# Performance work log

Hardware: AMD Instinct MI355X
Metric: run time of the kernel (lower is better)

Reference implementation:

```python
import jax, jax.numpy as jnp
import numpy as np

N = 50000
E = 800000
EQ = 200000
IN_DIM = 256
H1 = 256
H2 = 128
EA = 16


def _lrelu(x):
    return jax.nn.leaky_relu(x, negative_slope=0.01)


def gcn_conv(h, edge_index, W, b, num_nodes):
    # PyG GCNConv: add self-loops, symmetric normalization, out = A_hat (h W) + b
    row, col = edge_index[0], edge_index[1]
    loop = jnp.arange(num_nodes, dtype=row.dtype)
    row = jnp.concatenate([row, loop])
    col = jnp.concatenate([col, loop])
    deg = jax.ops.segment_sum(jnp.ones(row.shape[0], dtype=h.dtype), col, num_segments=num_nodes)
    dinv = jnp.where(deg > 0, jax.lax.rsqrt(deg), 0.0)
    norm = dinv[row] * dinv[col]                      # [E+N]
    hw = h @ W                                        # [N, out]
    msg = hw[row] * norm[:, None]                     # gather + scale
    out = jax.ops.segment_sum(msg, col, num_segments=num_nodes)
    return out + b


def gru_cell(x, h, Wih, Whh, bih, bhh):
    # torch.nn.GRUCell, gate order (r, z, n); Wih/Whh stored as [in, 3H]
    gi = x @ Wih + bih
    gh = h @ Whh + bhh
    ir, iz, inn = jnp.split(gi, 3, axis=1)
    hr, hz, hn = jnp.split(gh, 3, axis=1)
    r = jax.nn.sigmoid(ir + hr)
    z = jax.nn.sigmoid(iz + hz)
    n = jnp.tanh(inn + r * hn)
    return (1.0 - z) * n + z * h


def setup_inputs() -> dict:
    key = jax.random.key(0)
    ks = jax.random.split(key, 24)

    def gn(k, shape, scale=0.05):
        return (jax.random.normal(k, shape, dtype=jnp.float32) * scale)

    inp = {
        "x": jax.random.normal(ks[0], (N, IN_DIM), dtype=jnp.float32),
        "edge_index": jax.random.randint(ks[1], (2, E), 0, N, dtype=jnp.int32).astype(jnp.int64),
        "edge_label_index": jax.random.randint(ks[2], (2, EQ), 0, N, dtype=jnp.int32).astype(jnp.int64),
        "edge_attr": jax.random.normal(ks[3], (EQ, EA), dtype=jnp.float32),
        "prev1": jax.random.normal(ks[4], (N, H1), dtype=jnp.float32) * 0.1,
        "prev2": jax.random.normal(ks[5], (N, H2), dtype=jnp.float32) * 0.1,
        "pre1_W": gn(ks[6], (IN_DIM, 256)), "pre1_b": jnp.zeros((256,), jnp.float32),
        "pre2_W": gn(ks[7], (256, 128)), "pre2_b": jnp.zeros((128,), jnp.float32),
        "conv1_W": gn(ks[8], (128, H1)), "conv1_b": jnp.zeros((H1,), jnp.float32),
        "conv2_W": gn(ks[9], (H1, H2)), "conv2_b": jnp.zeros((H2,), jnp.float32),
        "gru1_Wih": gn(ks[10], (H1, 3 * H1)), "gru1_Whh": gn(ks[11], (H1, 3 * H1)),
        "gru1_bih": jnp.zeros((3 * H1,), jnp.float32), "gru1_bhh": jnp.zeros((3 * H1,), jnp.float32),
        "gru2_Wih": gn(ks[12], (H2, 3 * H2)), "gru2_Whh": gn(ks[13], (H2, 3 * H2)),
        "gru2_bih": jnp.zeros((3 * H2,), jnp.float32), "gru2_bhh": jnp.zeros((3 * H2,), jnp.float32),
        "post_W": gn(ks[14], (2 * H2 + EA, 1)), "post_b": jnp.zeros((1,), jnp.float32),
    }
    return inp


def reference(x, edge_index, edge_label_index, edge_attr, prev1, prev2,
              pre1_W, pre1_b, pre2_W, pre2_b,
              conv1_W, conv1_b, conv2_W, conv2_b,
              gru1_Wih, gru1_Whh, gru1_bih, gru1_bhh,
              gru2_Wih, gru2_Whh, gru2_bih, gru2_bhh,
              post_W, post_b):
    num_nodes = x.shape[0]
    # dense preprocessing (dropout p=0.0 -> identity)
    h = _lrelu(x @ pre1_W + pre1_b)
    h = _lrelu(h @ pre2_W + pre2_b)          # [N,128]
    # GCN layer 1 + GRU update with previous embeddings
    h = _lrelu(gcn_conv(h, edge_index, conv1_W, conv1_b, num_nodes))
    h = gru_cell(h, prev1, gru1_Wih, gru1_Whh, gru1_bih, gru1_bhh)
    emb1 = h
    # GCN layer 2 + GRU update
    h = _lrelu(gcn_conv(h, edge_index, conv2_W, conv2_b, num_nodes))
    h = gru_cell(h, prev2, gru2_Wih, gru2_Whh, gru2_bih, gru2_bhh)
    emb2 = h
    # edge-level prediction: gather endpoints, concat with edge_attr, linear
    h_src = h[edge_label_index[0]]
    h_dst = h[edge_label_index[1]]
    combined = jnp.concatenate([h_src, h_dst, edge_attr], axis=1)  # [Eq, 2*H2+EA]
    scores = (combined @ post_W + post_b).reshape(-1)              # [Eq]
    return (scores, emb1, emb2)
```

## Files before the change

kernel.cpp:

```cpp
#include <hip/hip_runtime.h>
#include <hip/hip_bf16.h>

#define DEVFN __device__ __forceinline__

constexpr int NN = 50000;
constexpr int NE = 800000;
constexpr int NQ = 200000;
constexpr long MP = 50048;

typedef __attribute__((ext_vector_type(8))) short bf16x8;
typedef __attribute__((ext_vector_type(2))) short s16x2;
typedef __attribute__((ext_vector_type(2))) float f32x2;
typedef __attribute__((ext_vector_type(4))) float f32x4;
typedef __attribute__((address_space(1))) const void gv_t;
typedef __attribute__((address_space(3))) void lv_t;

DEVFN float lrelu(float x) { return x > 0.f ? x : 0.01f * x; }
DEVFN float sigmoidf(float x) { return 1.f / (1.f + __expf(-x)); }
DEVFN float tanh_fast(float x) {
    float xc = fminf(fmaxf(x, -15.f), 15.f);
    float t = __expf(2.f * xc);
    return (t - 1.f) / (t + 1.f);
}

DEVFN short f2b(float v) {
    __hip_bfloat16 h = __float2bfloat16(v);
    return *reinterpret_cast<short*>(&h);
}
DEVFN float b2f(short s) {
    union { unsigned u; float f; } z;
    z.u = ((unsigned)(unsigned short)s) << 16;
    return z.f;
}
DEVFN void gld16(const void* g, void* l) {
    __builtin_amdgcn_global_load_lds((gv_t*)g, (lv_t*)l, 16, 0, 0);
}

#define WAITV4 asm volatile("s_waitcnt vmcnt(4)" ::: "memory")
#define WAITV0 asm volatile("s_waitcnt vmcnt(0)" ::: "memory")
#define CFENCE asm volatile("" ::: "memory")

DEVFN void swz_rc(int d, int nwg, int NC, int& rw, int& cs) {
    int q0 = nwg >> 3, rr = nwg & 7;
    int xcd = d & 7, idx = d >> 3;
    int w = (xcd < rr ? xcd * (q0 + 1) : rr * (q0 + 1) + (xcd - rr) * q0) + idx;
    rw = w / NC;
    cs = w - rw * NC;
}

template <int H>
DEVFN float gruw_val(const float* Wih, const float* Whh, int i) {
    constexpr int K2 = 2 * H, W3 = 3 * H;
    int np = i / K2, k = i % K2;
    int g16 = np >> 6, chunk = (np >> 4) & 3, cl = np & 15;
    int c = g16 * 16 + cl;
    if (chunk == 0) return (k < H) ? Wih[(long)k * W3 + c] : Whh[(long)(k - H) * W3 + c];
    if (chunk == 1) return (k < H) ? Wih[(long)k * W3 + H + c] : Whh[(long)(k - H) * W3 + H + c];
    if (chunk == 2) return (k < H) ? Wih[(long)k * W3 + 2 * H + c] : 0.f;
    return (k < H) ? 0.f : Whh[(long)(k - H) * W3 + 2 * H + c];
}

__global__ void prep_all(const float* __restrict__ x, const float* __restrict__ prev1,
                         const float* __restrict__ pre1W, const float* __restrict__ pre2W,
                         const float* __restrict__ conv1W, const float* __restrict__ conv2W,
                         const float* __restrict__ g1ih, const float* __restrict__ g1hh,
                         const float* __restrict__ g2ih, const float* __restrict__ g2hh,
                         short* __restrict__ xb, short* __restrict__ AP1,
                         short* __restrict__ pre1T, short* __restrict__ pre2T,
                         short* __restrict__ conv1T, short* __restrict__ conv2T,
                         short* __restrict__ W1g1, short* __restrict__ W1g2) {
    long i = (long)blockIdx.x * 256 + threadIdx.x;
    if (i < MP * 256) {
        xb[i] = (i < (long)NN * 256) ? f2b(x[i]) : (short)0;
        return;
    }
    i -= MP * 256;
    if (i < (long)NN * 256) {
        long r = i >> 8; int c = (int)(i & 255);
        AP1[r * 512 + 256 + c] = f2b(prev1[i]);
        return;
    }
    i -= (long)NN * 256;
    if (i < 65536) { int ii = (int)i, n = ii >> 8, k = ii & 255; pre1T[ii] = f2b(pre1W[k * 256 + n]); return; }
    i -= 65536;
    if (i < 32768) { int ii = (int)i, n = ii >> 8, k = ii & 255; pre2T[ii] = f2b(pre2W[k * 128 + n]); return; }
    i -= 32768;
    if (i < 32768) { int ii = (int)i, n = ii >> 7, k = ii & 127; conv1T[ii] = f2b(conv1W[k * 256 + n]); return; }
    i -= 32768;
    if (i < 32768) { int ii = (int)i, n = ii >> 8, k = ii & 255; conv2T[ii] = f2b(conv2W[k * 128 + n]); return; }
    i -= 32768;
    if (i < 524288) { W1g1[i] = f2b(gruw_val<256>(g1ih, g1hh, (int)i)); return; }
    i -= 524288;
    if (i < 131072) W1g2[i] = f2b(gruw_val<128>(g2ih, g2hh, (int)i));
}

template <int EPI, int K>
__global__ __launch_bounds__(256)
void gemm_mfma(const short* __restrict__ A, const short* __restrict__ Bt,
               const float* __restrict__ bias,
               short* __restrict__ Cb, int obS, int NC, int nwg) {
    constexpr int NS = K / 32;
    __shared__ alignas(16) short As[3][4096];
    __shared__ alignas(16) short Bs[3][4096];
    const int tid = threadIdx.x;
    const int lane = tid & 63, w = tid >> 6;
    const int wr = w >> 1, wc = w & 1;
    int rw, cs;
    swz_rc(blockIdx.x, nwg, NC, rw, cs);
    const long row0 = (long)rw * 128;
    const long col0 = (long)cs * 128;

    f32x4 acc[4][4] = {};

    const int kcs = ((tid & 3) ^ ((tid >> 3) & 3)) * 8;
    const short* gA = A + (row0 + (tid >> 2)) * (long)K + kcs;
    const short* gB = Bt + (col0 + (tid >> 2)) * (long)K + kcs;
    const long half = 64 * (long)K;

    auto stage = [&](int b, int k0) {
        gld16(gA + k0, &As[b][tid * 8]);
        gld16(gA + half + k0, &As[b][2048 + tid * 8]);
        gld16(gB + k0, &Bs[b][tid * 8]);
        gld16(gB + half + k0, &Bs[b][2048 + tid * 8]);
    };

    stage(0, 0);
    stage(1, 32);
    const int l15 = lane & 15;
    const int kq = ((lane >> 4) ^ ((l15 >> 1) & 3)) * 8;
#pragma unroll
    for (int t = 0; t < NS; ++t) {
        if (t + 1 < NS) { WAITV4; } else { WAITV0; }
        __builtin_amdgcn_s_barrier();
        CFENCE;
        if (t + 2 < NS) stage((t + 2) % 3, (t + 2) * 32);
        const int cur = t % 3;
        bf16x8 af[4], bfr[4];
#pragma unroll
        for (int i = 0; i < 4; ++i)
            af[i] = *(const bf16x8*)&As[cur][(wr * 64 + i * 16 + l15) * 32 + kq];
#pragma unroll
        for (int j = 0; j < 4; ++j)
            bfr[j] = *(const bf16x8*)&Bs[cur][(wc * 64 + j * 16 + l15) * 32 + kq];
#pragma unroll
        for (int i = 0; i < 4; ++i)
#pragma unroll
            for (int j = 0; j < 4; ++j)
                acc[i][j] = __builtin_amdgcn_mfma_f32_16x16x32_bf16(af[i], bfr[j], acc[i][j], 0, 0, 0);
    }

    const int cr = (lane >> 4) * 4, cc = lane & 15;
#pragma unroll
    for (int i = 0; i < 4; ++i) {
#pragma unroll
        for (int j = 0; j < 4; ++j) {
            const long col = col0 + wc * 64 + j * 16 + cc;
            float bv = (EPI == 1) ? bias[col] : 0.f;
#pragma unroll
            for (int r = 0; r < 4; ++r) {
                const long row = row0 + wr * 64 + i * 16 + cr + r;
                float v = acc[i][j][r];
                if (EPI == 1) v = lrelu(v + bv);
                Cb[row * obS + col] = f2b(v);
            }
        }
    }
}

template <int H, bool WRITEB>
__global__ __launch_bounds__(256)
void gru_wide(const short* __restrict__ AP, const short* __restrict__ W1,
              const float* __restrict__ prevf,
              const float* __restrict__ bih, const float* __restrict__ bhh,
              float* __restrict__ outF, short* __restrict__ outB, int M,
              int NC, int nwg) {
    constexpr int K2 = 2 * H;
    constexpr int NS = K2 / 32;
    __shared__ alignas(16) short As[3][4096];
    __shared__ alignas(16) short Bs[3][4096];
    const int tid = threadIdx.x;
    const int lane = tid & 63, w = tid >> 6;
    const int wr = w >> 1, wc = w & 1;
    int rw, cs;
    swz_rc(blockIdx.x, nwg, NC, rw, cs);
    const long row0 = (long)rw * 128;

    f32x4 acc[4][4] = {};

    const int kcs = ((tid & 3) ^ ((tid >> 3) & 3)) * 8;
    const short* gA = AP + (row0 + (tid >> 2)) * (long)K2 + kcs;
    const short* gB = W1 + ((long)cs * 128 + (tid >> 2)) * (long)K2 + kcs;
    const long half = 64 * (long)K2;

    auto stage = [&](int b, int k0) {
        gld16(gA + k0, &As[b][tid * 8]);
        gld16(gA + half + k0, &As[b][2048 + tid * 8]);
        gld16(gB + k0, &Bs[b][tid * 8]);
        gld16(gB + half + k0, &Bs[b][2048 + tid * 8]);
    };

    stage(0, 0);
    stage(1, 32);
    const int l15 = lane & 15;
    const int kq = ((lane >> 4) ^ ((l15 >> 1) & 3)) * 8;
#pragma unroll
    for (int t = 0; t < NS; ++t) {
        const bool lo = (t * 32 < H);
        if (t + 1 < NS) { WAITV4; } else { WAITV0; }
        __builtin_amdgcn_s_barrier();
        CFENCE;
        if (t + 2 < NS) stage((t + 2) % 3, (t + 2) * 32);
        const int cur = t % 3;
        bf16x8 af[4], bfr[4];
#pragma unroll
        for (int i = 0; i < 4; ++i)
            af[i] = *(const bf16x8*)&As[cur][(wr * 64 + i * 16 + l15) * 32 + kq];
#pragma unroll
        for (int j = 0; j < 4; ++j) {
            if ((j == 2 && !lo) || (j == 3 && lo)) continue;
            bfr[j] = *(const bf16x8*)&Bs[cur][(wc * 64 + j * 16 + l15) * 32 + kq];
        }
#pragma unroll
        for (int i = 0; i < 4; ++i)
#pragma unroll
            for (int j = 0; j < 4; ++j) {
                if ((j == 2 && !lo) || (j == 3 && lo)) continue;
                acc[i][j] = __builtin_amdgcn_mfma_f32_16x16x32_bf16(af[i], bfr[j], acc[i][j], 0, 0, 0);
            }
    }

    const int cr = (lane >> 4) * 4;
    const int c = cs * 32 + wc * 16 + (lane & 15);
    const float bsr = bih[c] + bhh[c];
    const float bsz = bih[H + c] + bhh[H + c];
    const float bin = bih[2 * H + c];
    const float bhn = bhh[2 * H + c];
#pragma unroll
    for (int i = 0; i < 4; ++i) {
#pragma unroll
        for (int r = 0; r < 4; ++r) {
            const long row = row0 + wr * 64 + i * 16 + cr + r;
            if (row >= M) continue;
            float rg = sigmoidf(acc[i][0][r] + bsr);
            float zg = sigmoidf(acc[i][1][r] + bsz);
            float ng = tanh_fast(acc[i][2][r] + bin + rg * (acc[i][3][r] + bhn));
            float o = (1.f - zg) * ng + zg * prevf[row * (long)H + c];
            outF[row * (long)H + c] = o;
            if (WRITEB) outB[row * (long)H + c] = f2b(o);
        }
    }
}

__global__ void cnt_kernel(const int* __restrict__ cols, int* __restrict__ cnt, int E) {
    int e = blockIdx.x * 256 + threadIdx.x;
    if (e < E) atomicAdd(&cnt[cols[e]], 1);
}

__global__ void scan1(const int* __restrict__ cnt, int* __restrict__ off,
                      int* __restrict__ bsum, float* __restrict__ dinv, int n) {
    __shared__ int sm[256];
    int i = blockIdx.x * 256 + threadIdx.x;
    int v = (i < n) ? cnt[i] : 0;
    if (i < n) dinv[i] = rsqrtf((float)v + 1.0f);
    sm[threadIdx.x] = v;
    __syncthreads();
    for (int s = 1; s < 256; s <<= 1) {
        int t = (threadIdx.x >= s) ? sm[threadIdx.x - s] : 0;
        __syncthreads();
        sm[threadIdx.x] += t;
        __syncthreads();
    }
    if (i < n) off[i + 1] = sm[threadIdx.x];
    if (threadIdx.x == 255) bsum[blockIdx.x] = sm[255];
}

__global__ void scan2(int* __restrict__ bsum, int nb) {
    __shared__ int sm[256];
    int v = (threadIdx.x < nb) ? bsum[threadIdx.x] : 0;
    sm[threadIdx.x] = v;
    __syncthreads();
    for (int s = 1; s < 256; s <<= 1) {
        int t = (threadIdx.x >= s) ? sm[threadIdx.x - s] : 0;
        __syncthreads();
        sm[threadIdx.x] += t;
        __syncthreads();
    }
    if (threadIdx.x < nb) bsum[threadIdx.x] = sm[threadIdx.x] - v;
}

__global__ void scan3(int* __restrict__ off, const int* __restrict__ bsum, int n) {
    int i = blockIdx.x * 256 + threadIdx.x;
    if (i < n) off[i + 1] += bsum[blockIdx.x];
    if (i == 0) off[0] = 0;
}

__global__ void fill_csr(const int* __restrict__ rows, const int* __restrict__ cols,
                         const float* __restrict__ dinv, const int* __restrict__ off,
                         int* __restrict__ cursor, int* __restrict__ srow,
                         float* __restrict__ snorm, int E) {
    int e = blockIdx.x * 256 + threadIdx.x;
    if (e >= E) return;
    int r = rows[e], c = cols[e];
    int p = off[c] + atomicAdd(&cursor[c], 1);
    srow[p] = r;
    snorm[p] = dinv[r] * dinv[c];
}

template <int OS, bool EPI, bool PREV>
__global__ __launch_bounds__(256)
void gather_agg(const short* __restrict__ hwb, const int* __restrict__ off,
                const int* __restrict__ srow, const float* __restrict__ snorm,
                const float* __restrict__ dinv, const float* __restrict__ bias,
                const float* __restrict__ prevf,
                short* __restrict__ aggb, int n) {
    constexpr int H = 128;
    int t = blockIdx.x * 256 + threadIdx.x;
    int c = t >> 6, l = t & 63;
    if (c >= n) return;
    const int fo = l * 2;
    float acc0, acc1;
    {
        float dd = dinv[c] * dinv[c];
        s16x2 v = *(const s16x2*)&hwb[(long)c * H + fo];
        acc0 = b2f(v[0]) * dd;
        acc1 = b2f(v[1]) * dd;
    }
    int e = off[c];
    const int e1 = off[c + 1];
    for (; e + 3 < e1; e += 4) {
        int r0 = srow[e], r1 = srow[e + 1], r2 = srow[e + 2], r3 = srow[e + 3];
        float n0 = snorm[e], n1 = snorm[e + 1], n2 = snorm[e + 2], n3 = snorm[e + 3];
        s16x2 v0 = *(const s16x2*)&hwb[(long)r0 * H + fo];
        s16x2 v1 = *(const s16x2*)&hwb[(long)r1 * H + fo];
        s16x2 v2 = *(const s16x2*)&hwb[(long)r2 * H + fo];
        s16x2 v3 = *(const s16x2*)&hwb[(long)r3 * H + fo];
        acc0 += b2f(v0[0]) * n0 + b2f(v1[0]) * n1 + b2f(v2[0]) * n2 + b2f(v3[0]) * n3;
        acc1 += b2f(v0[1]) * n0 + b2f(v1[1]) * n1 + b2f(v2[1]) * n2 + b2f(v3[1]) * n3;
    }
    for (; e < e1; ++e) {
        int r0 = srow[e];
        float n0 = snorm[e];
        s16x2 v0 = *(const s16x2*)&hwb[(long)r0 * H + fo];
        acc0 += b2f(v0[0]) * n0;
        acc1 += b2f(v0[1]) * n0;
    }
    s16x2 o;
    if (EPI) {
        o[0] = f2b(lrelu(acc0 + bias[fo]));
        o[1] = f2b(lrelu(acc1 + bias[fo + 1]));
    } else {
        o[0] = f2b(acc0);
        o[1] = f2b(acc1);
    }
    *(s16x2*)&aggb[(long)c * OS + fo] = o;
    if (PREV) {
        f32x2 p = *(const f32x2*)&prevf[(long)c * H + fo];
        s16x2 pb;
        pb[0] = f2b(p[0]);
        pb[1] = f2b(p[1]);
        *(s16x2*)&aggb[(long)c * OS + H + fo] = pb;
    }
}

__global__ void edge_score_b(const short* __restrict__ emb2b, const int* __restrict__ eli,
                             const float* __restrict__ ea, const float* __restrict__ pw,
                             const float* __restrict__ pb, float* __restrict__ scores, int Q) {
    int t = blockIdx.x * 256 + threadIdx.x;
    int e = t >> 6, l = t & 63;
    if (e >= Q) return;
    int s = eli[e], d = eli[Q + e];
    const int f = l * 2;
    s16x2 vs = *(const s16x2*)&emb2b[(long)s * 128 + f];
    s16x2 vd = *(const s16x2*)&emb2b[(long)d * 128 + f];
    float acc = b2f(vs[0]) * pw[f] + b2f(vs[1]) * pw[f + 1]
              + b2f(vd[0]) * pw[128 + f] + b2f(vd[1]) * pw[128 + f + 1];
    if (l < 16) acc += ea[(long)e * 16 + l] * pw[256 + l];
#pragma unroll
    for (int off = 32; off > 0; off >>= 1) acc += __shfl_down(acc, off);
    if (l == 0) scores[e] = acc + pb[0];
}


extern "C" void kernel_launch(void* const* d_in, const int* in_sizes, int n_in,
                              void* d_out, int out_size, void* d_ws, size_t ws_size,
                              hipStream_t stream) {
    const float* x       = (const float*)d_in[0];
    const int*   ei      = (const int*)d_in[1];
    const int*   eli     = (const int*)d_in[2];
    const float* eattr   = (const float*)d_in[3];
    const float* prev1   = (const float*)d_in[4];
    const float* prev2   = (const float*)d_in[5];
    const float* pre1_W  = (const float*)d_in[6];
    const float* pre1_b  = (const float*)d_in[7];
    const float* pre2_W  = (const float*)d_in[8];
    const float* pre2_b  = (const float*)d_in[9];
    const float* conv1_W = (const float*)d_in[10];
    const float* conv1_b = (const float*)d_in[11];
    const float* conv2_W = (const float*)d_in[12];
    const float* conv2_b = (const float*)d_in[13];
    const float* g1_Wih  = (const float*)d_in[14];
    const float* g1_Whh  = (const float*)d_in[15];
    const float* g1_bih  = (const float*)d_in[16];
    const float* g1_bhh  = (const float*)d_in[17];
    const float* g2_Wih  = (const float*)d_in[18];
    const float* g2_Whh  = (const float*)d_in[19];
    const float* g2_bih  = (const float*)d_in[20];
    const float* g2_bhh  = (const float*)d_in[21];
    const float* post_W  = (const float*)d_in[22];
    const float* post_b  = (const float*)d_in[23];

    float* out    = (float*)d_out;
    float* scores = out;
    float* emb1   = out + NQ;
    float* emb2   = emb1 + (long)NN * 256;

    char* ws = (char*)d_ws;
    const long S256 = MP * 256 * 2;
    const long S128 = MP * 128 * 2;
    short* R1  = (short*)ws;
    short* R2  = (short*)(ws + S256);
    short* R3  = (short*)(ws + 2 * S256);
    short* AP1 = (short*)(ws + 2 * S256 + S128);
    short* AP2 = R1;
    char*  wts = ws + 4 * S256 + S128;
    short* pre1T  = (short*)wts;
    short* pre2T  = pre1T + 256 * 256;
    short* conv1T = pre2T + 128 * 256;
    short* conv2T = conv1T + 256 * 128;
    short* W1g1   = conv2T + 128 * 256;
    short* W1g2   = W1g1 + 1024 * 512;
    float* dinv   = (float*)(W1g2 + 512 * 256);
    int*   cnt    = (int*)(dinv + NN);
    int*   cursor = cnt + NN;
    int*   off    = cursor + NN;
    int*   bsum   = off + NN + 1;
    int*   srow   = bsum + 256;
    float* snorm  = (float*)(srow + NE);

    const int* rows = ei;
    const int* cols = ei + NE;

    dim3 blk(256);
    const int NB = (NN + 255) / 256;

    const long PREP = MP * 256 + (long)NN * 256 + 65536 + 3 * 32768 + 524288 + 131072;
    prep_all<<<(int)((PREP + 255) / 256), blk, 0, stream>>>(
        x, prev1, pre1_W, pre2_W, conv1_W, conv2_W,
        g1_Wih, g1_Whh, g2_Wih, g2_Whh,
        R1, AP1, pre1T, pre2T, conv1T, conv2T, W1g1, W1g2);

    hipMemsetAsync(cnt, 0, 2 * NN * sizeof(int), stream);
    cnt_kernel<<<(NE + 255) / 256, blk, 0, stream>>>(cols, cnt, NE);
    scan1<<<NB, blk, 0, stream>>>(cnt, off, bsum, dinv, NN);
    scan2<<<1, blk, 0, stream>>>(bsum, NB);
    scan3<<<NB, blk, 0, stream>>>(off, bsum, NN);
    fill_csr<<<(NE + 255) / 256, blk, 0, stream>>>(rows, cols, dinv, off, cursor, srow, snorm, NE);

    gemm_mfma<1, 256><<<782, blk, 0, stream>>>(R1, pre1T, pre1_b, R2, 256, 2, 782);
    gemm_mfma<1, 256><<<391, blk, 0, stream>>>(R2, pre2T, pre2_b, R3, 128, 1, 391);

    gather_agg<128, false, false><<<(NN + 3) / 4, blk, 0, stream>>>(
        R3, off, srow, snorm, dinv, nullptr, nullptr, R1, NN);
    gemm_mfma<1, 128><<<782, blk, 0, stream>>>(R1, conv1T, conv1_b, AP1, 512, 2, 782);

    gru_wide<256, true><<<3128, blk, 0, stream>>>(AP1, W1g1, prev1, g1_bih, g1_bhh,
                                                  emb1, R2, NN, 8, 3128);

    gemm_mfma<0, 256><<<391, blk, 0, stream>>>(R2, conv2T, nullptr, R3, 128, 1, 391);

    gather_agg<256, true, true><<<(NN + 3) / 4, blk, 0, stream>>>(
        R3, off, srow, snorm, dinv, conv2_b, prev2, AP2, NN);

    gru_wide<128, true><<<1564, blk, 0, stream>>>(AP2, W1g2, prev2, g2_bih, g2_bhh,
                                                  emb2, R3, NN, 4, 1564);

    edge_score_b<<<NQ / 4, blk, 0, stream>>>(R3, eli, eattr, post_W, post_b, scores, NQ);
}
```

Baseline: 459.3 us.

## Precompute per-node post-linear dots and fold edge-degree counting into prep kernel

Edge scoring is split in two. A per-node pass computes the two dot products of emb2 with the src and dst halves of post_W, and a light per-edge kernel then adds the edge_attr dot and looks up two scalars instead of gathering two 128-wide rows per query edge. The degree-count atomics are also merged into the prep_all kernel, with the memset moved before it, which removes one launch. The cost is an extra pass over all nodes and two small workspace arrays. Since 200k query edges over 50k nodes means rows are re-gathered about eight times, the per-node dots should reduce gather traffic.

```diff
diff --git a/kernel.cpp b/kernel.cpp
--- a/kernel.cpp
+++ b/kernel.cpp
@@ -65,6 +65,7 @@
                          const float* __restrict__ conv1W, const float* __restrict__ conv2W,
                          const float* __restrict__ g1ih, const float* __restrict__ g1hh,
                          const float* __restrict__ g2ih, const float* __restrict__ g2hh,
+                         const int* __restrict__ cols, int* __restrict__ cnt,
                          short* __restrict__ xb, short* __restrict__ AP1,
                          short* __restrict__ pre1T, short* __restrict__ pre2T,
                          short* __restrict__ conv1T, short* __restrict__ conv2T,
@@ -81,6 +82,8 @@
         return;
     }
     i -= (long)NN * 256;
+    if (i < NE) { atomicAdd(&cnt[cols[i]], 1); return; }
+    i -= NE;
     if (i < 65536) { int ii = (int)i, n = ii >> 8, k = ii & 255; pre1T[ii] = f2b(pre1W[k * 256 + n]); return; }
     i -= 65536;
     if (i < 32768) { int ii = (int)i, n = ii >> 8, k = ii & 255; pre2T[ii] = f2b(pre2W[k * 128 + n]); return; }
@@ -249,11 +252,6 @@
             if (WRITEB) outB[row * (long)H + c] = f2b(o);
         }
     }
-}
-
-__global__ void cnt_kernel(const int* __restrict__ cols, int* __restrict__ cnt, int E) {
-    int e = blockIdx.x * 256 + threadIdx.x;
-    if (e < E) atomicAdd(&cnt[cols[e]], 1);
 }
 
 __global__ void scan1(const int* __restrict__ cnt, int* __restrict__ off,
@@ -362,22 +360,38 @@
     }
 }
 
-__global__ void edge_score_b(const short* __restrict__ emb2b, const int* __restrict__ eli,
-                             const float* __restrict__ ea, const float* __restrict__ pw,
-                             const float* __restrict__ pb, float* __restrict__ scores, int Q) {
+__global__ void node_dots(const short* __restrict__ emb2b, const float* __restrict__ pw,
+                          float* __restrict__ u, float* __restrict__ v, int n) {
     int t = blockIdx.x * 256 + threadIdx.x;
-    int e = t >> 6, l = t & 63;
+    int c = t >> 6, l = t & 63;
+    if (c >= n) return;
+    const int f = l * 2;
+    s16x2 e = *(const s16x2*)&emb2b[(long)c * 128 + f];
+    float e0 = b2f(e[0]), e1 = b2f(e[1]);
+    float ua = e0 * pw[f] + e1 * pw[f + 1];
+    float va = e0 * pw[128 + f] + e1 * pw[128 + f + 1];
+#pragma unroll
+    for (int off = 32; off > 0; off >>= 1) {
+        ua += __shfl_down(ua, off);
+        va += __shfl_down(va, off);
+    }
+    if (l == 0) { u[c] = ua; v[c] = va; }
+}
+
+__global__ void edge_lite(const int* __restrict__ eli, const float* __restrict__ ea,
+                          const float* __restrict__ pw, const float* __restrict__ pb,
+                          const float* __restrict__ u, const float* __restrict__ v,
+                          float* __restrict__ scores, int Q) {
+    int t = blockIdx.x * 256 + threadIdx.x;
+    int e = t >> 4, l = t & 15;
     if (e >= Q) return;
-    int s = eli[e], d = eli[Q + e];
-    const int f = l * 2;
-    s16x2 vs = *(const s16x2*)&emb2b[(long)s * 128 + f];
-    s16x2 vd = *(const s16x2*)&emb2b[(long)d * 128 + f];
-    float acc = b2f(vs[0]) * pw[f] + b2f(vs[1]) * pw[f + 1]
-              + b2f(vd[0]) * pw[128 + f] + b2f(vd[1]) * pw[128 + f + 1];
-    if (l < 16) acc += ea[(long)e * 16 + l] * pw[256 + l];
-#pragma unroll
-    for (int off = 32; off > 0; off >>= 1) acc += __shfl_down(acc, off);
-    if (l == 0) scores[e] = acc + pb[0];
+    float acc = ea[(long)e * 16 + l] * pw[256 + l];
+#pragma unroll
+    for (int off = 8; off > 0; off >>= 1) acc += __shfl_down(acc, off, 16);
+    if (l == 0) {
+        int s = eli[e], d = eli[Q + e];
+        scores[e] = acc + u[s] + v[d] + pb[0];
+    }
 }
 
 
@@ -436,6 +450,8 @@
     int*   bsum   = off + NN + 1;
     int*   srow   = bsum + 256;
     float* snorm  = (float*)(srow + NE);
+    float* uvec   = snorm + NE;
+    float* vvec   = uvec + NN;
 
     const int* rows = ei;
     const int* cols = ei + NE;
@@ -443,14 +459,13 @@
     dim3 blk(256);
     const int NB = (NN + 255) / 256;
 
-    const long PREP = MP * 256 + (long)NN * 256 + 65536 + 3 * 32768 + 524288 + 131072;
+    hipMemsetAsync(cnt, 0, 2 * NN * sizeof(int), stream);
+    const long PREP = MP * 256 + (long)NN * 256 + NE + 65536 + 3 * 32768 + 524288 + 131072;
     prep_all<<<(int)((PREP + 255) / 256), blk, 0, stream>>>(
         x, prev1, pre1_W, pre2_W, conv1_W, conv2_W,
-        g1_Wih, g1_Whh, g2_Wih, g2_Whh,
+        g1_Wih, g1_Whh, g2_Wih, g2_Whh, cols, cnt,
         R1, AP1, pre1T, pre2T, conv1T, conv2T, W1g1, W1g2);
 
-    hipMemsetAsync(cnt, 0, 2 * NN * sizeof(int), stream);
-    cnt_kernel<<<(NE + 255) / 256, blk, 0, stream>>>(cols, cnt, NE);
     scan1<<<NB, blk, 0, stream>>>(cnt, off, bsum, dinv, NN);
     scan2<<<1, blk, 0, stream>>>(bsum, NB);
     scan3<<<NB, blk, 0, stream>>>(off, bsum, NN);
@@ -474,5 +489,7 @@
     gru_wide<128, true><<<1564, blk, 0, stream>>>(AP2, W1g2, prev2, g2_bih, g2_bhh,
                                                   emb2, R3, NN, 4, 1564);
 
-    edge_score_b<<<NQ / 4, blk, 0, stream>>>(R3, eli, eattr, post_W, post_b, scores, NQ);
-}
+    node_dots<<<(NN + 3) / 4, blk, 0, stream>>>(R3, post_W, uvec, vvec, NN);
+    edge_lite<<<(NQ + 15) / 16, blk, 0, stream>>>(eli, eattr, post_W, post_b,
+                                                  uvec, vvec, scores, NQ);
+}
```

New measurement: 433.2 us. -5.7%, faster.
